# Kernel optimization log

Hardware: AMD Instinct MI355X
Metric: run time of the kernel (lower is better)

## Reference

```python
import jax, jax.numpy as jnp
import numpy as np

H, E, DFF = 768, 8, 3072
B, S = 2, 1024


def setup_inputs() -> dict:
    key = jax.random.key(0)
    ks = jax.random.split(key, 4)
    scale = 1.0 / np.sqrt(H)
    return {
        "x": jax.random.normal(ks[0], (B, S, H), dtype=jnp.float32),
        "Wg": jax.random.normal(ks[1], (H, E), dtype=jnp.float32) * scale,
        "bg": jnp.zeros((E,), dtype=jnp.float32),
        "W1": jax.random.normal(ks[2], (E, H, DFF), dtype=jnp.float32) * scale,
        "b1": jnp.zeros((E, DFF), dtype=jnp.float32),
        "W2": jax.random.normal(ks[3], (E, DFF, H), dtype=jnp.float32) * (1.0 / np.sqrt(DFF)),
        "b2": jnp.zeros((E, H), dtype=jnp.float32),
        "top_k": 2,
    }


def reference(x, Wg, bg, W1, b1, W2, b2, top_k):
    b, s, h = x.shape
    xf = x.reshape(-1, h)                       # [T, H]
    logits = xf @ Wg + bg                        # [T, E]
    probs = jax.nn.softmax(logits, axis=-1)
    w, idx = jax.lax.top_k(probs, top_k)         # [T, K]
    w = w / jnp.sum(w, axis=-1, keepdims=True)   # renormalize top-k weights
    # dense combine weights per (token, expert): [T, E]
    comb = jnp.sum(jax.nn.one_hot(idx, W1.shape[0], dtype=xf.dtype) * w[..., None], axis=1)
    # per-expert MLP: Linear -> exact GELU -> Linear
    hmid = jax.nn.gelu(jnp.einsum('th,ehf->etf', xf, W1) + b1[:, None, :], approximate=False)
    eo = jnp.einsum('etf,efh->eth', hmid, W2) + b2[:, None, :]   # [E, T, H]
    out = jnp.einsum('te,eth->th', comb, eo)     # weighted combine
    return out.reshape(b, s, h)
```

## Files before the change

### kernel.cpp

```cpp
#include <hip/hip_runtime.h>
#include <hip/hip_bf16.h>
#include <math.h>

#define H_DIM 768
#define E_NUM 8
#define DFF   3072
#define T_NUM 2048
#define PAIRS 4096

typedef __attribute__((ext_vector_type(8))) short          s16x8;
typedef __attribute__((ext_vector_type(4))) float          f32x4;
typedef __attribute__((ext_vector_type(4))) unsigned int   u32x4;
typedef __attribute__((ext_vector_type(4))) unsigned short u16x4;
typedef __attribute__((ext_vector_type(8))) unsigned short u16x8;

__device__ __forceinline__ unsigned short f2bf(float f) {
  unsigned int u = __builtin_bit_cast(unsigned int, f);
  u += 0x7FFFu + ((u >> 16) & 1u);
  return (unsigned short)(u >> 16);
}

__device__ __forceinline__ float bf2f(unsigned short v) {
  unsigned int u = ((unsigned int)v) << 16;
  return __builtin_bit_cast(float, u);
}

__device__ __forceinline__ float gelu_fast(float x) {
  float t = x * x;
  float a = __builtin_fmaf(t, -0.10294221f, -2.3022082f);
  float w;
  asm("v_exp_f32 %0, %1" : "=v"(w) : "v"(x * a));
  float r;
  float d = 1.0f + w;
  asm("v_rcp_f32 %0, %1" : "=v"(r) : "v"(d));
  return x * r;
}

__global__ __launch_bounds__(256) void k_route(
    const float* __restrict__ x, const float* __restrict__ Wg,
    const float* __restrict__ bg, int* __restrict__ eidx, float* __restrict__ ew) {
  int wave = threadIdx.x >> 6, lane = threadIdx.x & 63;
  int t = blockIdx.x * 4 + wave;
  const float* xr = x + (size_t)t * H_DIM;
  float acc[E_NUM];
#pragma unroll
  for (int e = 0; e < E_NUM; ++e) acc[e] = 0.f;
#pragma unroll
  for (int i = 0; i < H_DIM / 64; ++i) {
    int h = i * 64 + lane;
    float xv = xr[h];
    f32x4 w0 = *(const f32x4*)&Wg[h * 8];
    f32x4 w1 = *(const f32x4*)&Wg[h * 8 + 4];
    acc[0] += xv * w0[0]; acc[1] += xv * w0[1];
    acc[2] += xv * w0[2]; acc[3] += xv * w0[3];
    acc[4] += xv * w1[0]; acc[5] += xv * w1[1];
    acc[6] += xv * w1[2]; acc[7] += xv * w1[3];
  }
#pragma unroll
  for (int e = 0; e < E_NUM; ++e) {
#pragma unroll
    for (int off = 32; off > 0; off >>= 1) acc[e] += __shfl_xor(acc[e], off);
  }
  if (lane == 0) {
    float l[E_NUM];
#pragma unroll
    for (int e = 0; e < E_NUM; ++e) l[e] = acc[e] + bg[e];
    int i0 = 0;
#pragma unroll
    for (int e = 1; e < E_NUM; ++e) if (l[e] > l[i0]) i0 = e;
    int i1 = (i0 == 0) ? 1 : 0;
#pragma unroll
    for (int e = 0; e < E_NUM; ++e) if (e != i0 && l[e] > l[i1]) i1 = e;
    float d  = expf(l[i1] - l[i0]);
    eidx[2 * t]     = i0;
    eidx[2 * t + 1] = i1;
    ew[2 * t]       = 1.f / (1.f + d);
    ew[2 * t + 1]   = d / (1.f + d);
  }
}

__global__ __launch_bounds__(256) void k_build(
    const int* __restrict__ eidx, int* __restrict__ counts, int* __restrict__ offsets,
    int* __restrict__ tok_of, int* __restrict__ slot_of) {
  __shared__ int cnt[E_NUM];
  __shared__ int cur[E_NUM];
  int tid = threadIdx.x;
  if (tid < E_NUM) cnt[tid] = 0;
  __syncthreads();
#pragma unroll
  for (int i = 0; i < PAIRS / 256; ++i)
    atomicAdd(&cnt[eidx[i * 256 + tid]], 1);
  __syncthreads();
  if (tid == 0) {
    int s = 0;
    for (int e = 0; e < E_NUM; ++e) { cur[e] = s; s += cnt[e]; }
  }
  __syncthreads();
  if (tid < E_NUM) { counts[tid] = cnt[tid]; offsets[tid] = cur[tid]; }
#pragma unroll
  for (int i = 0; i < PAIRS / 256; ++i) {
    int p = i * 256 + tid;
    int s = atomicAdd(&cur[eidx[p]], 1);
    tok_of[s] = p >> 1;
    slot_of[p] = s;
  }
}

__global__ void k_gather(const float* __restrict__ x, const int* __restrict__ tok_of,
                         unsigned short* __restrict__ Xg) {
  int s = blockIdx.x;
  int lane = threadIdx.x;
  int t = tok_of[s];
  const f32x4* xr = (const f32x4*)(x + (size_t)t * H_DIM);
  u16x4* orow = (u16x4*)(Xg + (size_t)s * H_DIM);
#pragma unroll
  for (int i = 0; i < H_DIM / 256; ++i) {
    f32x4 v = xr[i * 64 + lane];
    u16x4 o;
    o[0] = f2bf(v[0]); o[1] = f2bf(v[1]); o[2] = f2bf(v[2]); o[3] = f2bf(v[3]);
    orow[i * 64 + lane] = o;
  }
}

__global__ __launch_bounds__(256) void k_transpose_cast(
    const float* __restrict__ in, unsigned short* __restrict__ out, int R, int C) {
  __shared__ unsigned short tile[64][72];
  int e  = blockIdx.z;
  int c0 = blockIdx.x * 64, r0 = blockIdx.y * 64;
  const float* ip = in + (size_t)e * R * C;
  unsigned short* op = out + (size_t)e * R * C;
  int tid = threadIdx.x;
  int tx = tid & 15, ty = tid >> 4;
#pragma unroll
  for (int i = 0; i < 4; ++i) {
    int r = ty + 16 * i;
    f32x4 v = *(const f32x4*)&ip[(size_t)(r0 + r) * C + c0 + tx * 4];
    u16x4 o;
    o[0] = f2bf(v[0]); o[1] = f2bf(v[1]); o[2] = f2bf(v[2]); o[3] = f2bf(v[3]);
    *(u16x4*)&tile[r][tx * 4] = o;
  }
  __syncthreads();
  int c  = tid & 63;
  int rc = (tid >> 6) * 16;
#pragma unroll
  for (int h = 0; h < 2; ++h) {
    u16x8 o;
#pragma unroll
    for (int j = 0; j < 8; ++j) o[j] = tile[rc + h * 8 + j][c];
    *(u16x8*)&op[(size_t)(c0 + c) * R + r0 + rc + h * 8] = o;
  }
}

template <int KTOT, int NT, int NSPLIT, int MT_MAX, bool GELU_OUT>
__global__ __launch_bounds__(256) void k_gemm(
    const unsigned short* __restrict__ A, const unsigned short* __restrict__ B,
    const float* __restrict__ bias, void* __restrict__ C,
    const int* __restrict__ counts, const int* __restrict__ offsets) {
  constexpr int NDIM  = NT * 128;
  constexpr int KLEN  = KTOT / NSPLIT;
  constexpr int NSTEP = KLEN / 64;
  constexpr int TOT   = NT * NSPLIT * MT_MAX * E_NUM;
  int b = blockIdx.x;
  int l = (b & 7) * (TOT / 8) + (b >> 3);
  int mt = l % MT_MAX;  l /= MT_MAX;
  int part = l % NSPLIT; l /= NSPLIT;
  int nt = l % NT;
  int e  = l / NT;
  int Me = counts[e];
  if (mt * 128 >= Me) return;
  int seg = offsets[e];

  __shared__ __align__(16) unsigned short Al[2][128 * 64];
  __shared__ __align__(16) unsigned short Bl[2][128 * 64];

  int tid  = threadIdx.x;
  int lane = tid & 63;
  int wave = tid >> 6;
  int wm = wave >> 1, wn = wave & 1;

  int sr   = tid >> 3;
  int scl  = (tid & 7) * 8;
  int scs  = (((tid & 7) ^ (sr & 7)) * 8);
  int rxor = (lane & 7) << 3;

  f32x4 acc[4][4];
#pragma unroll
  for (int m = 0; m < 4; ++m)
#pragma unroll
    for (int n = 0; n < 4; ++n) acc[m][n] = (f32x4){0.f, 0.f, 0.f, 0.f};

  const unsigned short* Abase = A + (size_t)seg * KTOT;
  const unsigned short* Bbase = B + (size_t)e * NDIM * KTOT + (size_t)(nt * 128) * KTOT;
  const int kbeg = part * KLEN;

  auto stage = [&](int bb, int k0) {
#pragma unroll
    for (int j = 0; j < 4; ++j) {
      int row = j * 32 + sr;
      int r = mt * 128 + row;
      r = (r < Me) ? r : (Me - 1);
      const unsigned short* gp = Abase + (size_t)r * KTOT + k0 + scs;
      __builtin_amdgcn_global_load_lds(
          (__attribute__((address_space(1))) void*)gp,
          (__attribute__((address_space(3))) void*)&Al[bb][row * 64 + scl], 16, 0, 0);
    }
#pragma unroll
    for (int j = 0; j < 4; ++j) {
      int row = j * 32 + sr;
      const unsigned short* gp = Bbase + (size_t)row * KTOT + k0 + scs;
      __builtin_amdgcn_global_load_lds(
          (__attribute__((address_space(1))) void*)gp,
          (__attribute__((address_space(3))) void*)&Bl[bb][row * 64 + scl], 16, 0, 0);
    }
  };

  auto compute = [&](int bb) {
#pragma unroll
    for (int kk = 0; kk < 2; ++kk) {
      int ko = kk * 32 + (lane >> 4) * 8;
      s16x8 af[4], bfr[4];
#pragma unroll
      for (int m = 0; m < 4; ++m) {
        int row = wm * 64 + m * 16 + (lane & 15);
        u32x4 v = *(const u32x4*)&Al[bb][(row * 64 + ko) ^ rxor];
        af[m] = __builtin_bit_cast(s16x8, v);
      }
#pragma unroll
      for (int n = 0; n < 4; ++n) {
        int row = wn * 64 + n * 16 + (lane & 15);
        u32x4 v = *(const u32x4*)&Bl[bb][(row * 64 + ko) ^ rxor];
        bfr[n] = __builtin_bit_cast(s16x8, v);
      }
#pragma unroll
      for (int m = 0; m < 4; ++m)
#pragma unroll
        for (int n = 0; n < 4; ++n)
          acc[m][n] = __builtin_amdgcn_mfma_f32_16x16x32_bf16(af[m], bfr[n], acc[m][n], 0, 0, 0);
    }
  };

  stage(0, kbeg);
  stage(1, kbeg + 64);
  int cur = 0;
#pragma unroll
  for (int s = 0; s < NSTEP; ++s) {
    if (s + 1 < NSTEP) asm volatile("s_waitcnt vmcnt(8)" ::: "memory");
    else               asm volatile("s_waitcnt vmcnt(0)" ::: "memory");
    __builtin_amdgcn_s_barrier();
    compute(cur);
    if (s + 2 < NSTEP) {
      __builtin_amdgcn_s_barrier();
      stage(cur, kbeg + (s + 2) * 64);
    }
    cur ^= 1;
  }

  int rbase = mt * 128 + wm * 64;
  int cbase = nt * 128 + wn * 64;
#pragma unroll
  for (int m = 0; m < 4; ++m) {
#pragma unroll
    for (int n = 0; n < 4; ++n) {
      int col = cbase + n * 16 + (lane & 15);
      float bv = GELU_OUT ? bias[e * NDIM + col] : 0.f;
#pragma unroll
      for (int r = 0; r < 4; ++r) {
        int row = rbase + m * 16 + (lane >> 4) * 4 + r;
        if (row < Me) {
          float v = acc[m][n][r] + bv;
          size_t idx = ((size_t)part * PAIRS + seg + row) * NDIM + col;
          if constexpr (GELU_OUT) {
            ((unsigned short*)C)[idx] = f2bf(gelu_fast(v));
          } else {
            ((unsigned short*)C)[idx] = f2bf(v);
          }
        }
      }
    }
  }
}

template <int NSPLIT>
__global__ void k_combine(const unsigned short* __restrict__ P, const int* __restrict__ slot_of,
                          const int* __restrict__ eidx, const float* __restrict__ ew,
                          const float* __restrict__ b2, float* __restrict__ out) {
  int t = blockIdx.x;
  int i = threadIdx.x;
  int s0 = slot_of[2 * t], s1 = slot_of[2 * t + 1];
  int e0 = eidx[2 * t],    e1 = eidx[2 * t + 1];
  float w0 = ew[2 * t], w1 = ew[2 * t + 1];
  f32x4 a = *(const f32x4*)&b2[e0 * H_DIM + i * 4];
  f32x4 c = *(const f32x4*)&b2[e1 * H_DIM + i * 4];
#pragma unroll
  for (int p = 0; p < NSPLIT; ++p) {
    u16x4 va = *(const u16x4*)&P[((size_t)p * PAIRS + s0) * H_DIM + i * 4];
    u16x4 vb = *(const u16x4*)&P[((size_t)p * PAIRS + s1) * H_DIM + i * 4];
#pragma unroll
    for (int j = 0; j < 4; ++j) { a[j] += bf2f(va[j]); c[j] += bf2f(vb[j]); }
  }
  f32x4 o;
  o[0] = w0 * a[0] + w1 * c[0];
  o[1] = w0 * a[1] + w1 * c[1];
  o[2] = w0 * a[2] + w1 * c[2];
  o[3] = w0 * a[3] + w1 * c[3];
  ((f32x4*)(out + (size_t)t * H_DIM))[i] = o;
}

extern "C" void kernel_launch(void* const* d_in, const int* in_sizes, int n_in,
                              void* d_out, int out_size, void* d_ws, size_t ws_size,
                              hipStream_t stream) {
  (void)in_sizes; (void)n_in; (void)out_size;
  const float* x  = (const float*)d_in[0];
  const float* Wg = (const float*)d_in[1];
  const float* bg = (const float*)d_in[2];
  const float* W1 = (const float*)d_in[3];
  const float* b1 = (const float*)d_in[4];
  const float* W2 = (const float*)d_in[5];
  const float* b2 = (const float*)d_in[6];
  float* out = (float*)d_out;

  char* w = (char*)d_ws;
  size_t off = 0;
  auto take = [&](size_t n) { void* p = w + off; off = (off + n + 255) & ~(size_t)255; return p; };
  int*   ctrl    = (int*)  take(64 * sizeof(int));
  int*   eidx    = (int*)  take(PAIRS * sizeof(int));
  float* ew      = (float*)take(PAIRS * sizeof(float));
  int*   slot_of = (int*)  take(PAIRS * sizeof(int));
  int*   tok_of  = (int*)  take(PAIRS * sizeof(int));
  unsigned short* Xg   = (unsigned short*)take((size_t)PAIRS * H_DIM * 2);
  unsigned short* Wb   = (unsigned short*)take((size_t)E_NUM * H_DIM * DFF * 2);
  unsigned short* Hmid = (unsigned short*)take((size_t)PAIRS * DFF * 2);
  size_t p_off = off;
  unsigned short* P = (unsigned short*)(w + p_off);
  bool split4 = (p_off + (size_t)4 * PAIRS * H_DIM * 2) <= ws_size;
  if (p_off + (size_t)PAIRS * H_DIM * 2 > ws_size) return;

  int* counts  = ctrl;
  int* offsets = ctrl + 8;

  k_route<<<T_NUM / 4, 256, 0, stream>>>(x, Wg, bg, eidx, ew);
  k_build<<<1, 256, 0, stream>>>(eidx, counts, offsets, tok_of, slot_of);
  k_gather<<<PAIRS, 64, 0, stream>>>(x, tok_of, Xg);

  k_transpose_cast<<<dim3(DFF / 64, H_DIM / 64, E_NUM), 256, 0, stream>>>(W1, Wb, H_DIM, DFF);
  k_gemm<H_DIM, DFF / 128, 1, 8, true><<<(DFF / 128) * E_NUM * 8, 256, 0, stream>>>(
      Xg, Wb, b1, Hmid, counts, offsets);

  k_transpose_cast<<<dim3(H_DIM / 64, DFF / 64, E_NUM), 256, 0, stream>>>(W2, Wb, DFF, H_DIM);

  if (split4) {
    k_gemm<DFF, H_DIM / 128, 4, 8, false><<<(H_DIM / 128) * E_NUM * 4 * 8, 256, 0, stream>>>(
        Hmid, Wb, b2, P, counts, offsets);
    k_combine<4><<<T_NUM, 192, 0, stream>>>(P, slot_of, eidx, ew, b2, out);
  } else {
    k_gemm<DFF, H_DIM / 128, 1, 8, false><<<(H_DIM / 128) * E_NUM * 8, 256, 0, stream>>>(
        Hmid, Wb, b2, P, counts, offsets);
    k_combine<1><<<T_NUM, 192, 0, stream>>>(P, slot_of, eidx, ew, b2, out);
  }
}
```

Measured before the change: 169.9 us.

## Fuse weight transposes into routing and first GEMM launches to overlap work

Merges routing with the W1 transpose-cast into one launch, and the first expert GEMM with the W2 transpose-cast into another. Each merged kernel splits its blocks between the two jobs by block index, so independent work runs concurrently and fills idle CUs instead of running as separate serial launches. W2 gets its own workspace buffer so it no longer overwrites W1, and the GEMM block ordering is remapped (nt fastest, then expert). LDS becomes dynamic at 64KB for the fused GEMM kernel, which may lower occupancy for the transpose blocks that share it. The split-4 path is now always used.

```diff
diff --git a/kernel.cpp b/kernel.cpp
--- a/kernel.cpp
+++ b/kernel.cpp
@@ -36,11 +36,12 @@
   return x * r;
 }
 
-__global__ __launch_bounds__(256) void k_route(
-    const float* __restrict__ x, const float* __restrict__ Wg,
+
+__device__ __forceinline__ void route_body(
+    int rb, const float* __restrict__ x, const float* __restrict__ Wg,
     const float* __restrict__ bg, int* __restrict__ eidx, float* __restrict__ ew) {
   int wave = threadIdx.x >> 6, lane = threadIdx.x & 63;
-  int t = blockIdx.x * 4 + wave;
+  int t = rb * 4 + wave;
   const float* xr = x + (size_t)t * H_DIM;
   float acc[E_NUM];
 #pragma unroll
@@ -79,54 +80,15 @@
   }
 }
 
-__global__ __launch_bounds__(256) void k_build(
-    const int* __restrict__ eidx, int* __restrict__ counts, int* __restrict__ offsets,
-    int* __restrict__ tok_of, int* __restrict__ slot_of) {
-  __shared__ int cnt[E_NUM];
-  __shared__ int cur[E_NUM];
-  int tid = threadIdx.x;
-  if (tid < E_NUM) cnt[tid] = 0;
-  __syncthreads();
-#pragma unroll
-  for (int i = 0; i < PAIRS / 256; ++i)
-    atomicAdd(&cnt[eidx[i * 256 + tid]], 1);
-  __syncthreads();
-  if (tid == 0) {
-    int s = 0;
-    for (int e = 0; e < E_NUM; ++e) { cur[e] = s; s += cnt[e]; }
-  }
-  __syncthreads();
-  if (tid < E_NUM) { counts[tid] = cnt[tid]; offsets[tid] = cur[tid]; }
-#pragma unroll
-  for (int i = 0; i < PAIRS / 256; ++i) {
-    int p = i * 256 + tid;
-    int s = atomicAdd(&cur[eidx[p]], 1);
-    tok_of[s] = p >> 1;
-    slot_of[p] = s;
-  }
-}
-
-__global__ void k_gather(const float* __restrict__ x, const int* __restrict__ tok_of,
-                         unsigned short* __restrict__ Xg) {
-  int s = blockIdx.x;
-  int lane = threadIdx.x;
-  int t = tok_of[s];
-  const f32x4* xr = (const f32x4*)(x + (size_t)t * H_DIM);
-  u16x4* orow = (u16x4*)(Xg + (size_t)s * H_DIM);
-#pragma unroll
-  for (int i = 0; i < H_DIM / 256; ++i) {
-    f32x4 v = xr[i * 64 + lane];
-    u16x4 o;
-    o[0] = f2bf(v[0]); o[1] = f2bf(v[1]); o[2] = f2bf(v[2]); o[3] = f2bf(v[3]);
-    orow[i * 64 + lane] = o;
-  }
-}
-
-__global__ __launch_bounds__(256) void k_transpose_cast(
-    const float* __restrict__ in, unsigned short* __restrict__ out, int R, int C) {
-  __shared__ unsigned short tile[64][72];
-  int e  = blockIdx.z;
-  int c0 = blockIdx.x * 64, r0 = blockIdx.y * 64;
+__device__ __forceinline__ void transpose_body(
+    char* smem, int tb, const float* __restrict__ in, unsigned short* __restrict__ out,
+    int R, int C) {
+  unsigned short (*tile)[72] = (unsigned short (*)[72])smem;
+  int e   = tb / ((R / 64) * (C / 64));
+  int rem = tb % ((R / 64) * (C / 64));
+  int bx  = rem % (C / 64);
+  int by  = rem / (C / 64);
+  int c0 = bx * 64, r0 = by * 64;
   const float* ip = in + (size_t)e * R * C;
   unsigned short* op = out + (size_t)e * R * C;
   int tid = threadIdx.x;
@@ -152,26 +114,25 @@
 }
 
 template <int KTOT, int NT, int NSPLIT, int MT_MAX, bool GELU_OUT>
-__global__ __launch_bounds__(256) void k_gemm(
+__device__ __forceinline__ void gemm_body(
+    char* smem, int blk,
     const unsigned short* __restrict__ A, const unsigned short* __restrict__ B,
     const float* __restrict__ bias, void* __restrict__ C,
     const int* __restrict__ counts, const int* __restrict__ offsets) {
   constexpr int NDIM  = NT * 128;
   constexpr int KLEN  = KTOT / NSPLIT;
   constexpr int NSTEP = KLEN / 64;
-  constexpr int TOT   = NT * NSPLIT * MT_MAX * E_NUM;
-  int b = blockIdx.x;
-  int l = (b & 7) * (TOT / 8) + (b >> 3);
-  int mt = l % MT_MAX;  l /= MT_MAX;
-  int part = l % NSPLIT; l /= NSPLIT;
-  int nt = l % NT;
-  int e  = l / NT;
+  int l = blk;
+  int nt = l % NT;  l /= NT;
+  int e  = l & 7;   l >>= 3;
+  int part = l % NSPLIT;
+  int mt = l / NSPLIT;
   int Me = counts[e];
   if (mt * 128 >= Me) return;
   int seg = offsets[e];
 
-  __shared__ __align__(16) unsigned short Al[2][128 * 64];
-  __shared__ __align__(16) unsigned short Bl[2][128 * 64];
+  unsigned short* Al = (unsigned short*)smem;
+  unsigned short* Bl = (unsigned short*)(smem + 2 * 128 * 64 * 2);
 
   int tid  = threadIdx.x;
   int lane = tid & 63;
@@ -202,7 +163,8 @@
       const unsigned short* gp = Abase + (size_t)r * KTOT + k0 + scs;
       __builtin_amdgcn_global_load_lds(
           (__attribute__((address_space(1))) void*)gp,
-          (__attribute__((address_space(3))) void*)&Al[bb][row * 64 + scl], 16, 0, 0);
+          (__attribute__((address_space(3))) void*)&Al[bb * 128 * 64 + row * 64 + scl],
+          16, 0, 0);
     }
 #pragma unroll
     for (int j = 0; j < 4; ++j) {
@@ -210,7 +172,8 @@
       const unsigned short* gp = Bbase + (size_t)row * KTOT + k0 + scs;
       __builtin_amdgcn_global_load_lds(
           (__attribute__((address_space(1))) void*)gp,
-          (__attribute__((address_space(3))) void*)&Bl[bb][row * 64 + scl], 16, 0, 0);
+          (__attribute__((address_space(3))) void*)&Bl[bb * 128 * 64 + row * 64 + scl],
+          16, 0, 0);
     }
   };
 
@@ -222,13 +185,13 @@
 #pragma unroll
       for (int m = 0; m < 4; ++m) {
         int row = wm * 64 + m * 16 + (lane & 15);
-        u32x4 v = *(const u32x4*)&Al[bb][(row * 64 + ko) ^ rxor];
+        u32x4 v = *(const u32x4*)&Al[(bb * 128 * 64) + ((row * 64 + ko) ^ rxor)];
         af[m] = __builtin_bit_cast(s16x8, v);
       }
 #pragma unroll
       for (int n = 0; n < 4; ++n) {
         int row = wn * 64 + n * 16 + (lane & 15);
-        u32x4 v = *(const u32x4*)&Bl[bb][(row * 64 + ko) ^ rxor];
+        u32x4 v = *(const u32x4*)&Bl[(bb * 128 * 64) + ((row * 64 + ko) ^ rxor)];
         bfr[n] = __builtin_bit_cast(s16x8, v);
       }
 #pragma unroll
@@ -280,6 +243,94 @@
   }
 }
 
+
+__global__ __launch_bounds__(256) void k_route_t1(
+    const float* __restrict__ x, const float* __restrict__ Wg,
+    const float* __restrict__ bg, int* __restrict__ eidx, float* __restrict__ ew,
+    const float* __restrict__ W1, unsigned short* __restrict__ Wb1) {
+  extern __shared__ char smem[];
+  int b = blockIdx.x;
+  if (b % 10 == 0) route_body(b / 10, x, Wg, bg, eidx, ew);
+  else             transpose_body(smem, b - b / 10 - 1, W1, Wb1, H_DIM, DFF);
+}
+
+__global__ __launch_bounds__(256) void k_gemm1_t2(
+    const unsigned short* __restrict__ Xg, const unsigned short* __restrict__ Wb1,
+    const float* __restrict__ b1, unsigned short* __restrict__ Hmid,
+    const int* __restrict__ counts, const int* __restrict__ offsets,
+    const float* __restrict__ W2, unsigned short* __restrict__ Wb2) {
+  extern __shared__ char smem[];
+  int b = blockIdx.x;
+  if ((b & 3) == 0)
+    gemm_body<H_DIM, DFF / 128, 1, 8, true>(smem, b >> 2, Xg, Wb1, b1, Hmid, counts, offsets);
+  else
+    transpose_body(smem, b - (b >> 2) - 1, W2, Wb2, DFF, H_DIM);
+}
+
+__global__ __launch_bounds__(256) void k_route(
+    const float* __restrict__ x, const float* __restrict__ Wg,
+    const float* __restrict__ bg, int* __restrict__ eidx, float* __restrict__ ew) {
+  route_body(blockIdx.x, x, Wg, bg, eidx, ew);
+}
+
+__global__ __launch_bounds__(256) void k_transpose_cast(
+    const float* __restrict__ in, unsigned short* __restrict__ out, int R, int C) {
+  extern __shared__ char smem[];
+  transpose_body(smem, blockIdx.x, in, out, R, C);
+}
+
+template <int KTOT, int NT, int NSPLIT, int MT_MAX, bool GELU_OUT>
+__global__ __launch_bounds__(256) void k_gemm(
+    const unsigned short* __restrict__ A, const unsigned short* __restrict__ B,
+    const float* __restrict__ bias, void* __restrict__ C,
+    const int* __restrict__ counts, const int* __restrict__ offsets) {
+  extern __shared__ char smem[];
+  gemm_body<KTOT, NT, NSPLIT, MT_MAX, GELU_OUT>(smem, blockIdx.x, A, B, bias, C, counts, offsets);
+}
+
+__global__ __launch_bounds__(256) void k_build(
+    const int* __restrict__ eidx, int* __restrict__ counts, int* __restrict__ offsets,
+    int* __restrict__ tok_of, int* __restrict__ slot_of) {
+  __shared__ int cnt[E_NUM];
+  __shared__ int cur[E_NUM];
+  int tid = threadIdx.x;
+  if (tid < E_NUM) cnt[tid] = 0;
+  __syncthreads();
+#pragma unroll
+  for (int i = 0; i < PAIRS / 256; ++i)
+    atomicAdd(&cnt[eidx[i * 256 + tid]], 1);
+  __syncthreads();
+  if (tid == 0) {
+    int s = 0;
+    for (int e = 0; e < E_NUM; ++e) { cur[e] = s; s += cnt[e]; }
+  }
+  __syncthreads();
+  if (tid < E_NUM) { counts[tid] = cnt[tid]; offsets[tid] = cur[tid]; }
+#pragma unroll
+  for (int i = 0; i < PAIRS / 256; ++i) {
+    int p = i * 256 + tid;
+    int s = atomicAdd(&cur[eidx[p]], 1);
+    tok_of[s] = p >> 1;
+    slot_of[p] = s;
+  }
+}
+
+__global__ void k_gather(const float* __restrict__ x, const int* __restrict__ tok_of,
+                         unsigned short* __restrict__ Xg) {
+  int s = blockIdx.x;
+  int lane = threadIdx.x;
+  int t = tok_of[s];
+  const f32x4* xr = (const f32x4*)(x + (size_t)t * H_DIM);
+  u16x4* orow = (u16x4*)(Xg + (size_t)s * H_DIM);
+#pragma unroll
+  for (int i = 0; i < H_DIM / 256; ++i) {
+    f32x4 v = xr[i * 64 + lane];
+    u16x4 o;
+    o[0] = f2bf(v[0]); o[1] = f2bf(v[1]); o[2] = f2bf(v[2]); o[3] = f2bf(v[3]);
+    orow[i * 64 + lane] = o;
+  }
+}
+
 template <int NSPLIT>
 __global__ void k_combine(const unsigned short* __restrict__ P, const int* __restrict__ slot_of,
                           const int* __restrict__ eidx, const float* __restrict__ ew,
@@ -319,6 +370,9 @@
   const float* b2 = (const float*)d_in[6];
   float* out = (float*)d_out;
 
+  constexpr int TR_LDS   = 64 * 72 * 2;
+  constexpr int GEMM_LDS = 65536;
+
   char* w = (char*)d_ws;
   size_t off = 0;
   auto take = [&](size_t n) { void* p = w + off; off = (off + n + 255) & ~(size_t)255; return p; };
@@ -328,33 +382,36 @@
   int*   slot_of = (int*)  take(PAIRS * sizeof(int));
   int*   tok_of  = (int*)  take(PAIRS * sizeof(int));
   unsigned short* Xg   = (unsigned short*)take((size_t)PAIRS * H_DIM * 2);
-  unsigned short* Wb   = (unsigned short*)take((size_t)E_NUM * H_DIM * DFF * 2);
   unsigned short* Hmid = (unsigned short*)take((size_t)PAIRS * DFF * 2);
-  size_t p_off = off;
-  unsigned short* P = (unsigned short*)(w + p_off);
-  bool split4 = (p_off + (size_t)4 * PAIRS * H_DIM * 2) <= ws_size;
-  if (p_off + (size_t)PAIRS * H_DIM * 2 > ws_size) return;
+  unsigned short* P    = (unsigned short*)take((size_t)4 * PAIRS * H_DIM * 2);
+  unsigned short* Wb1  = (unsigned short*)take((size_t)E_NUM * H_DIM * DFF * 2);
+  size_t off_one = off;
+  unsigned short* Wb2  = (unsigned short*)take((size_t)E_NUM * H_DIM * DFF * 2);
+  bool fused = (off <= ws_size);
+  if (off_one > ws_size) return;
+  if (!fused) Wb2 = Wb1;
 
   int* counts  = ctrl;
   int* offsets = ctrl + 8;
 
-  k_route<<<T_NUM / 4, 256, 0, stream>>>(x, Wg, bg, eidx, ew);
-  k_build<<<1, 256, 0, stream>>>(eidx, counts, offsets, tok_of, slot_of);
-  k_gather<<<PAIRS, 64, 0, stream>>>(x, tok_of, Xg);
-
-  k_transpose_cast<<<dim3(DFF / 64, H_DIM / 64, E_NUM), 256, 0, stream>>>(W1, Wb, H_DIM, DFF);
-  k_gemm<H_DIM, DFF / 128, 1, 8, true><<<(DFF / 128) * E_NUM * 8, 256, 0, stream>>>(
-      Xg, Wb, b1, Hmid, counts, offsets);
-
-  k_transpose_cast<<<dim3(H_DIM / 64, DFF / 64, E_NUM), 256, 0, stream>>>(W2, Wb, DFF, H_DIM);
-
-  if (split4) {
-    k_gemm<DFF, H_DIM / 128, 4, 8, false><<<(H_DIM / 128) * E_NUM * 4 * 8, 256, 0, stream>>>(
-        Hmid, Wb, b2, P, counts, offsets);
-    k_combine<4><<<T_NUM, 192, 0, stream>>>(P, slot_of, eidx, ew, b2, out);
+  if (fused) {
+    k_route_t1<<<5120, 256, TR_LDS, stream>>>(x, Wg, bg, eidx, ew, W1, Wb1);
+    k_build<<<1, 256, 0, stream>>>(eidx, counts, offsets, tok_of, slot_of);
+    k_gather<<<PAIRS, 64, 0, stream>>>(x, tok_of, Xg);
+    k_gemm1_t2<<<6144, 256, GEMM_LDS, stream>>>(Xg, Wb1, b1, Hmid, counts, offsets, W2, Wb2);
   } else {
-    k_gemm<DFF, H_DIM / 128, 1, 8, false><<<(H_DIM / 128) * E_NUM * 8, 256, 0, stream>>>(
-        Hmid, Wb, b2, P, counts, offsets);
-    k_combine<1><<<T_NUM, 192, 0, stream>>>(P, slot_of, eidx, ew, b2, out);
-  }
-}
+    k_route<<<T_NUM / 4, 256, 0, stream>>>(x, Wg, bg, eidx, ew);
+    k_build<<<1, 256, 0, stream>>>(eidx, counts, offsets, tok_of, slot_of);
+    k_gather<<<PAIRS, 64, 0, stream>>>(x, tok_of, Xg);
+    k_transpose_cast<<<E_NUM * (H_DIM / 64) * (DFF / 64), 256, TR_LDS, stream>>>(
+        W1, Wb1, H_DIM, DFF);
+    k_gemm<H_DIM, DFF / 128, 1, 8, true><<<(DFF / 128) * E_NUM * 8, 256, GEMM_LDS, stream>>>(
+        Xg, Wb1, b1, Hmid, counts, offsets);
+    k_transpose_cast<<<E_NUM * (DFF / 64) * (H_DIM / 64), 256, TR_LDS, stream>>>(
+        W2, Wb2, DFF, H_DIM);
+  }
+
+  k_gemm<DFF, H_DIM / 128, 4, 8, false><<<(H_DIM / 128) * E_NUM * 4 * 8, 256, GEMM_LDS, stream>>>(
+      Hmid, Wb2, b2, P, counts, offsets);
+  k_combine<4><<<T_NUM, 192, 0, stream>>>(P, slot_of, eidx, ew, b2, out);
+}
```

New measurement: 250.0 us. +47.1%, slower.

## Fuse weight transposes into routing and gather kernels, change GEMM block order and split-K

Applied to the files above, without the earlier changes.

Routing is merged with the W1 transpose-cast into one launch, and the token gather with the W2 transpose-cast into another, so independent work shares a grid and there are fewer launches and serial gaps. W1 and W2 get separate bf16 buffers so the W2 conversion can run before the first GEMM. The GEMM block index now iterates over N tiles first and then experts, instead of the earlier XCD-strided mapping, and the second GEMM uses a 3-way K split instead of 4, which shrinks the partial-sum buffer and the combine reads. The cost is more workspace, and the fused kernels make every block reserve the transpose's shared-memory tile, even the routing and gather blocks.

```diff
diff --git a/kernel.cpp b/kernel.cpp
--- a/kernel.cpp
+++ b/kernel.cpp
@@ -36,11 +36,12 @@
   return x * r;
 }
 
-__global__ __launch_bounds__(256) void k_route(
-    const float* __restrict__ x, const float* __restrict__ Wg,
+
+__device__ __forceinline__ void route_body(
+    int rb, const float* __restrict__ x, const float* __restrict__ Wg,
     const float* __restrict__ bg, int* __restrict__ eidx, float* __restrict__ ew) {
   int wave = threadIdx.x >> 6, lane = threadIdx.x & 63;
-  int t = blockIdx.x * 4 + wave;
+  int t = rb * 4 + wave;
   const float* xr = x + (size_t)t * H_DIM;
   float acc[E_NUM];
 #pragma unroll
@@ -79,6 +80,75 @@
   }
 }
 
+__device__ __forceinline__ void transpose_body(
+    int tb, const float* __restrict__ in, unsigned short* __restrict__ out,
+    int R, int C) {
+  __shared__ unsigned short tile[64][72];
+  int e   = tb / ((R / 64) * (C / 64));
+  int rem = tb % ((R / 64) * (C / 64));
+  int bx  = rem % (C / 64);
+  int by  = rem / (C / 64);
+  int c0 = bx * 64, r0 = by * 64;
+  const float* ip = in + (size_t)e * R * C;
+  unsigned short* op = out + (size_t)e * R * C;
+  int tid = threadIdx.x;
+  int tx = tid & 15, ty = tid >> 4;
+#pragma unroll
+  for (int i = 0; i < 4; ++i) {
+    int r = ty + 16 * i;
+    f32x4 v = *(const f32x4*)&ip[(size_t)(r0 + r) * C + c0 + tx * 4];
+    u16x4 o;
+    o[0] = f2bf(v[0]); o[1] = f2bf(v[1]); o[2] = f2bf(v[2]); o[3] = f2bf(v[3]);
+    *(u16x4*)&tile[r][tx * 4] = o;
+  }
+  __syncthreads();
+  int c  = tid & 63;
+  int rc = (tid >> 6) * 16;
+#pragma unroll
+  for (int h = 0; h < 2; ++h) {
+    u16x8 o;
+#pragma unroll
+    for (int j = 0; j < 8; ++j) o[j] = tile[rc + h * 8 + j][c];
+    *(u16x8*)&op[(size_t)(c0 + c) * R + r0 + rc + h * 8] = o;
+  }
+}
+
+__device__ __forceinline__ void gather_body(
+    int gb, const float* __restrict__ x, const int* __restrict__ tok_of,
+    unsigned short* __restrict__ Xg) {
+  int s = gb * 4 + (threadIdx.x >> 6);
+  int lane = threadIdx.x & 63;
+  int t = tok_of[s];
+  const f32x4* xr = (const f32x4*)(x + (size_t)t * H_DIM);
+  u16x4* orow = (u16x4*)(Xg + (size_t)s * H_DIM);
+#pragma unroll
+  for (int i = 0; i < H_DIM / 256; ++i) {
+    f32x4 v = xr[i * 64 + lane];
+    u16x4 o;
+    o[0] = f2bf(v[0]); o[1] = f2bf(v[1]); o[2] = f2bf(v[2]); o[3] = f2bf(v[3]);
+    orow[i * 64 + lane] = o;
+  }
+}
+
+
+__global__ __launch_bounds__(256) void k_route_t1(
+    const float* __restrict__ x, const float* __restrict__ Wg,
+    const float* __restrict__ bg, int* __restrict__ eidx, float* __restrict__ ew,
+    const float* __restrict__ W1, unsigned short* __restrict__ Wb1) {
+  int b = blockIdx.x;
+  if (b < T_NUM / 4) route_body(b, x, Wg, bg, eidx, ew);
+  else               transpose_body(b - T_NUM / 4, W1, Wb1, H_DIM, DFF);
+}
+
+__global__ __launch_bounds__(256) void k_gather_t2(
+    const float* __restrict__ x, const int* __restrict__ tok_of,
+    unsigned short* __restrict__ Xg,
+    const float* __restrict__ W2, unsigned short* __restrict__ Wb2) {
+  int b = blockIdx.x;
+  if (b < PAIRS / 4) gather_body(b, x, tok_of, Xg);
+  else               transpose_body(b - PAIRS / 4, W2, Wb2, DFF, H_DIM);
+}
+
 __global__ __launch_bounds__(256) void k_build(
     const int* __restrict__ eidx, int* __restrict__ counts, int* __restrict__ offsets,
     int* __restrict__ tok_of, int* __restrict__ slot_of) {
@@ -106,51 +176,6 @@
   }
 }
 
-__global__ void k_gather(const float* __restrict__ x, const int* __restrict__ tok_of,
-                         unsigned short* __restrict__ Xg) {
-  int s = blockIdx.x;
-  int lane = threadIdx.x;
-  int t = tok_of[s];
-  const f32x4* xr = (const f32x4*)(x + (size_t)t * H_DIM);
-  u16x4* orow = (u16x4*)(Xg + (size_t)s * H_DIM);
-#pragma unroll
-  for (int i = 0; i < H_DIM / 256; ++i) {
-    f32x4 v = xr[i * 64 + lane];
-    u16x4 o;
-    o[0] = f2bf(v[0]); o[1] = f2bf(v[1]); o[2] = f2bf(v[2]); o[3] = f2bf(v[3]);
-    orow[i * 64 + lane] = o;
-  }
-}
-
-__global__ __launch_bounds__(256) void k_transpose_cast(
-    const float* __restrict__ in, unsigned short* __restrict__ out, int R, int C) {
-  __shared__ unsigned short tile[64][72];
-  int e  = blockIdx.z;
-  int c0 = blockIdx.x * 64, r0 = blockIdx.y * 64;
-  const float* ip = in + (size_t)e * R * C;
-  unsigned short* op = out + (size_t)e * R * C;
-  int tid = threadIdx.x;
-  int tx = tid & 15, ty = tid >> 4;
-#pragma unroll
-  for (int i = 0; i < 4; ++i) {
-    int r = ty + 16 * i;
-    f32x4 v = *(const f32x4*)&ip[(size_t)(r0 + r) * C + c0 + tx * 4];
-    u16x4 o;
-    o[0] = f2bf(v[0]); o[1] = f2bf(v[1]); o[2] = f2bf(v[2]); o[3] = f2bf(v[3]);
-    *(u16x4*)&tile[r][tx * 4] = o;
-  }
-  __syncthreads();
-  int c  = tid & 63;
-  int rc = (tid >> 6) * 16;
-#pragma unroll
-  for (int h = 0; h < 2; ++h) {
-    u16x8 o;
-#pragma unroll
-    for (int j = 0; j < 8; ++j) o[j] = tile[rc + h * 8 + j][c];
-    *(u16x8*)&op[(size_t)(c0 + c) * R + r0 + rc + h * 8] = o;
-  }
-}
-
 template <int KTOT, int NT, int NSPLIT, int MT_MAX, bool GELU_OUT>
 __global__ __launch_bounds__(256) void k_gemm(
     const unsigned short* __restrict__ A, const unsigned short* __restrict__ B,
@@ -159,13 +184,11 @@
   constexpr int NDIM  = NT * 128;
   constexpr int KLEN  = KTOT / NSPLIT;
   constexpr int NSTEP = KLEN / 64;
-  constexpr int TOT   = NT * NSPLIT * MT_MAX * E_NUM;
-  int b = blockIdx.x;
-  int l = (b & 7) * (TOT / 8) + (b >> 3);
-  int mt = l % MT_MAX;  l /= MT_MAX;
-  int part = l % NSPLIT; l /= NSPLIT;
-  int nt = l % NT;
-  int e  = l / NT;
+  int l = blockIdx.x;
+  int nt = l % NT;  l /= NT;
+  int e  = l & 7;   l >>= 3;
+  int part = l % NSPLIT;
+  int mt = l / NSPLIT;
   int Me = counts[e];
   if (mt * 128 >= Me) return;
   int seg = offsets[e];
@@ -328,33 +351,25 @@
   int*   slot_of = (int*)  take(PAIRS * sizeof(int));
   int*   tok_of  = (int*)  take(PAIRS * sizeof(int));
   unsigned short* Xg   = (unsigned short*)take((size_t)PAIRS * H_DIM * 2);
-  unsigned short* Wb   = (unsigned short*)take((size_t)E_NUM * H_DIM * DFF * 2);
   unsigned short* Hmid = (unsigned short*)take((size_t)PAIRS * DFF * 2);
-  size_t p_off = off;
-  unsigned short* P = (unsigned short*)(w + p_off);
-  bool split4 = (p_off + (size_t)4 * PAIRS * H_DIM * 2) <= ws_size;
-  if (p_off + (size_t)PAIRS * H_DIM * 2 > ws_size) return;
+  unsigned short* P    = (unsigned short*)take((size_t)3 * PAIRS * H_DIM * 2);
+  unsigned short* Wb1  = (unsigned short*)take((size_t)E_NUM * H_DIM * DFF * 2);
+  unsigned short* Wb2  = (unsigned short*)take((size_t)E_NUM * H_DIM * DFF * 2);
+  if (off > ws_size) return;
 
   int* counts  = ctrl;
   int* offsets = ctrl + 8;
 
-  k_route<<<T_NUM / 4, 256, 0, stream>>>(x, Wg, bg, eidx, ew);
+  k_route_t1<<<T_NUM / 4 + E_NUM * (H_DIM / 64) * (DFF / 64), 256, 0, stream>>>(
+      x, Wg, bg, eidx, ew, W1, Wb1);
   k_build<<<1, 256, 0, stream>>>(eidx, counts, offsets, tok_of, slot_of);
-  k_gather<<<PAIRS, 64, 0, stream>>>(x, tok_of, Xg);
-
-  k_transpose_cast<<<dim3(DFF / 64, H_DIM / 64, E_NUM), 256, 0, stream>>>(W1, Wb, H_DIM, DFF);
+  k_gather_t2<<<PAIRS / 4 + E_NUM * (DFF / 64) * (H_DIM / 64), 256, 0, stream>>>(
+      x, tok_of, Xg, W2, Wb2);
+
   k_gemm<H_DIM, DFF / 128, 1, 8, true><<<(DFF / 128) * E_NUM * 8, 256, 0, stream>>>(
-      Xg, Wb, b1, Hmid, counts, offsets);
-
-  k_transpose_cast<<<dim3(H_DIM / 64, DFF / 64, E_NUM), 256, 0, stream>>>(W2, Wb, DFF, H_DIM);
-
-  if (split4) {
-    k_gemm<DFF, H_DIM / 128, 4, 8, false><<<(H_DIM / 128) * E_NUM * 4 * 8, 256, 0, stream>>>(
-        Hmid, Wb, b2, P, counts, offsets);
-    k_combine<4><<<T_NUM, 192, 0, stream>>>(P, slot_of, eidx, ew, b2, out);
-  } else {
-    k_gemm<DFF, H_DIM / 128, 1, 8, false><<<(H_DIM / 128) * E_NUM * 8, 256, 0, stream>>>(
-        Hmid, Wb, b2, P, counts, offsets);
-    k_combine<1><<<T_NUM, 192, 0, stream>>>(P, slot_of, eidx, ew, b2, out);
-  }
-}
+      Xg, Wb1, b1, Hmid, counts, offsets);
+
+  k_gemm<DFF, H_DIM / 128, 3, 8, false><<<(H_DIM / 128) * E_NUM * 3 * 8, 256, 0, stream>>>(
+      Hmid, Wb2, b2, P, counts, offsets);
+  k_combine<3><<<T_NUM, 192, 0, stream>>>(P, slot_of, eidx, ew, b2, out);
+}
```

New measurement: 152.0 us. 10.5% less time.
